# Optimization experiments

Hardware: AMD Instinct MI355X
Metric: run time of the kernel (lower is better)

The kernel has to match this reference:

```python
import jax, jax.numpy as jnp
import numpy as np

EPS = 1e-8


def setup_inputs() -> dict:
    key = jax.random.key(0)
    k1, k2 = jax.random.split(key)
    B, C, L = 16, 4, 4096
    K, S = 256, 128
    x = jax.random.normal(k1, (B, C, L), dtype=jnp.float32)
    shapelets = jax.random.normal(k2, (C, K, S), dtype=jnp.float32)
    return {"x": x, "shapelets": shapelets}


def reference(x, shapelets):
    # x: (B, C, L); shapelets: (C, K, S)
    B, C, L = x.shape
    _, K, S = shapelets.shape
    W = L - S + 1  # number of sliding windows

    # unfold: (B, C, W, S) sliding windows with stride 1
    idx = jnp.arange(W)[:, None] + jnp.arange(S)[None, :]  # (W, S)
    win = x[:, :, idx]  # (B, C, W, S)
    win = win / jnp.maximum(jnp.linalg.norm(win, axis=-1, keepdims=True), EPS)

    shp = shapelets / jnp.maximum(
        jnp.linalg.norm(shapelets, axis=-1, keepdims=True), EPS
    )  # (C, K, S)

    # pairwise dot products: (B, C, W, K)
    sim = jnp.einsum("bcws,cks->bcwk", win, shp)
    # sum over channels, keepdim, transpose(2,3), divide by n_dims
    sim = jnp.sum(sim, axis=1, keepdims=True) / C  # (B, 1, W, K)
    sim = jnp.transpose(sim, (0, 1, 3, 2))  # (B, 1, K, W)
    sim = jax.nn.relu(sim)
    # global max-pool over window positions -> (B, 1, K)
    return jnp.max(sim, axis=3)
```

## Files before the change

### kernel.cpp

```cpp
#include <hip/hip_runtime.h>
#include <hip/hip_bf16.h>

#define NB 16
#define NC 4
#define NL 4096
#define NK 256
#define NS 128
#define NW (NL - NS + 1)
#define WPB 128
#define NWT ((NW + WPB - 1) / WPB)
#define KPB 64
#define EPSF 1e-8f

typedef __attribute__((ext_vector_type(8))) short bf16x8;
typedef __attribute__((ext_vector_type(4))) float floatx4;

typedef __attribute__((address_space(3))) unsigned int* lds_ptr_t;
typedef const __attribute__((address_space(1))) unsigned int* gbl_ptr_t;

__device__ inline short f2bf(float f) {
    __hip_bfloat16 h = __float2bfloat16(f);
    short s;
    __builtin_memcpy(&s, &h, sizeof(short));
    return s;
}

__device__ inline void gload_lds16(const void* g, void* l) {
    __builtin_amdgcn_global_load_lds((gbl_ptr_t)g, (lds_ptr_t)l, 16, 0, 0);
}

__global__ __launch_bounds__(64)
void norm_shp_kernel(const float* __restrict__ shp, short* __restrict__ shpn) {
    int ck = blockIdx.x;
    int k = ck & (NK - 1);
    int lane = threadIdx.x;
    const float* p = shp + (size_t)ck * NS;
    float v0 = p[lane];
    float v1 = p[lane + 64];
    float ss = v0 * v0 + v1 * v1;
    #pragma unroll
    for (int o = 32; o > 0; o >>= 1) ss += __shfl_xor(ss, o, 64);
    float rn = 1.f / fmaxf(sqrtf(ss), EPSF);
    int s0 = lane, s1 = lane + 64;
    int d0 = ((((s0 >> 3) ^ (k & 15)) << 3) | (s0 & 7));
    int d1 = ((((s1 >> 3) ^ (k & 15)) << 3) | (s1 & 7));
    shpn[(size_t)ck * NS + d0] = f2bf(v0 * rn);
    shpn[(size_t)ck * NS + d1] = f2bf(v1 * rn);
}

__global__ __launch_bounds__(256, 2)
void mcs_main_kernel(const float* __restrict__ x,
                     const short* __restrict__ shpn,
                     float* __restrict__ out) {
    __shared__ bf16x8 bs[NC][KPB * 16];
    __shared__ alignas(16) short xcp[NC][4][264];
    __shared__ alignas(16) float scratch[NC][264];
    __shared__ float invw[NC][WPB];

    const int kq = blockIdx.x, slot = blockIdx.y;
    const int tid = threadIdx.x;
    const int lane = tid & 63, wv = tid >> 6;
    const int m = lane & 15, q = lane >> 4, r = m & 3;
    const int kh = wv & 1, wh = wv >> 1;

    float xv[16];
    #pragma unroll
    for (int t = 0; t < 4; t++) {
        const int idx = slot * 4 + t;
        const int wt = idx & 31, b = idx >> 5;
        const int g = wt * WPB + tid;
        #pragma unroll
        for (int c = 0; c < NC; c++)
            xv[t * 4 + c] = (g < NL) ? x[((size_t)b * NC + c) * NL + g] : 0.f;
    }
    {
        const char* gbase = (const char*)shpn + (size_t)(kq * KPB) * NS * 2;
        #pragma unroll
        for (int c = 0; c < NC; c++) {
            const char* gc = gbase + (size_t)c * NK * NS * 2;
            char* lc = (char*)&bs[c][0];
            #pragma unroll
            for (int i = 0; i < 4; i++) {
                int off = (wv * 4 + i) * 1024;
                gload_lds16(gc + off + lane * 16, lc + off);
            }
        }
    }

    float res[4];

    #pragma unroll
    for (int t = 0; t < 4; t++) {
        const int idx = slot * 4 + t;
        const int wt = idx & 31;
        const int w0 = wt * WPB;

        #pragma unroll
        for (int c = 0; c < NC; c++) {
            float xf = xv[t * 4 + c];
            short hv = f2bf(xf);
            #pragma unroll
            for (int rr = 0; rr < 4; rr++) {
                int o2 = tid - rr;
                if (o2 >= 0) xcp[c][rr][o2] = hv;
            }
            scratch[c][tid] = xf * xf;
        }
        __syncthreads();

        {
            float4 v = *(const float4*)&scratch[wv][lane * 4];
            v.y += v.x; v.z += v.y; v.w += v.z;
            float tt = v.w;
            #pragma unroll
            for (int o = 1; o < 64; o <<= 1) {
                float u = __shfl_up(tt, o, 64);
                if (lane >= o) tt += u;
            }
            float excl = tt - v.w;
            v.x += excl; v.y += excl; v.z += excl; v.w += excl;
            *(float4*)&scratch[wv][lane * 4] = v;
        }
        __syncthreads();

        #pragma unroll
        for (int i = 0; i < 2; i++) {
            int ii = tid + 256 * i;
            int c = ii >> 7, o = ii & 127;
            float nn = scratch[c][o + 127] - (o ? scratch[c][o - 1] : 0.f);
            int w = w0 + o;
            invw[c][o] = (w < NW) ? 1.f / fmaxf(sqrtf(fmaxf(nn, 0.f)), EPSF)
                                  : 0.f;
        }
        if (t == 0) asm volatile("s_waitcnt vmcnt(0)" ::: "memory");
        __syncthreads();

        floatx4 tot[4][2];
        #pragma unroll
        for (int mt = 0; mt < 4; mt++)
            #pragma unroll
            for (int kt = 0; kt < 2; kt++)
                tot[mt][kt] = (floatx4){0.f, 0.f, 0.f, 0.f};

        #pragma unroll
        for (int c = 0; c < NC; c++) {
            floatx4 part[4][2];
            #pragma unroll
            for (int s0 = 0; s0 < NS; s0 += 32) {
                bf16x8 a[4];
                #pragma unroll
                for (int mt = 0; mt < 4; mt++) {
                    int ts = wh * 64 + mt * 16 + m + s0 + q * 8;
                    const uint2* pp = (const uint2*)&xcp[c][r][ts - r];
                    union { uint2 uu[2]; bf16x8 v; } cv;
                    cv.uu[0] = pp[0]; cv.uu[1] = pp[1];
                    a[mt] = cv.v;
                }
                int cc = (s0 >> 3) + q;
                #pragma unroll
                for (int kt = 0; kt < 2; kt++) {
                    int k = kh * 32 + kt * 16 + m;
                    bf16x8 bf = bs[c][(k << 4) | (cc ^ m)];
                    #pragma unroll
                    for (int mt = 0; mt < 4; mt++) {
                        part[mt][kt] = (s0 == 0)
                            ? __builtin_amdgcn_mfma_f32_16x16x32_bf16(
                                  a[mt], bf, (floatx4){0.f,0.f,0.f,0.f}, 0,0,0)
                            : __builtin_amdgcn_mfma_f32_16x16x32_bf16(
                                  a[mt], bf, part[mt][kt], 0, 0, 0);
                    }
                }
            }
            #pragma unroll
            for (int mt = 0; mt < 4; mt++) {
                const float4 iv =
                    *(const float4*)&invw[c][wh * 64 + mt * 16 + q * 4];
                floatx4 ivv = (floatx4){iv.x, iv.y, iv.z, iv.w};
                #pragma unroll
                for (int kt = 0; kt < 2; kt++) tot[mt][kt] += ivv * part[mt][kt];
            }
        }

        #pragma unroll
        for (int kt = 0; kt < 2; kt++) {
            floatx4 v0 = tot[0][kt], v1 = tot[1][kt],
                    v2 = tot[2][kt], v3 = tot[3][kt];
            float mx = fmaxf(fmaxf(fmaxf(v0.x, v0.y), fmaxf(v0.z, v0.w)),
                             fmaxf(fmaxf(v1.x, v1.y), fmaxf(v1.z, v1.w)));
            mx = fmaxf(mx, fmaxf(fmaxf(fmaxf(v2.x, v2.y), fmaxf(v2.z, v2.w)),
                                 fmaxf(fmaxf(v3.x, v3.y), fmaxf(v3.z, v3.w))));
            mx = fmaxf(mx, __shfl_xor(mx, 16, 64));
            mx = fmaxf(mx, __shfl_xor(mx, 32, 64));
            if (lane < 16) scratch[wv][kt * 16 + lane] = mx;
        }
        __syncthreads();
        if (tid < 64) {
            int khh = tid >> 5, j = tid & 31;
            float v = fmaxf(scratch[khh][j], scratch[khh + 2][j]);
            res[t] = fmaxf(v, 0.f) * 0.25f;
        }
        __syncthreads();
    }

    if (tid < 64) {
        int khh = tid >> 5, j = tid & 31;
        int kg = kq * KPB + khh * 32 + j;
        #pragma unroll
        for (int t = 0; t < 4; t++) {
            int b = (slot * 4 + t) >> 5;
            atomicMax((int*)out + (size_t)b * NK + kg, __float_as_int(res[t]));
        }
    }
}

extern "C" void kernel_launch(void* const* d_in, const int* in_sizes, int n_in,
                              void* d_out, int out_size, void* d_ws, size_t ws_size,
                              hipStream_t stream) {
    (void)in_sizes; (void)n_in; (void)out_size; (void)ws_size;
    const float* x   = (const float*)d_in[0];
    const float* shp = (const float*)d_in[1];
    float* out = (float*)d_out;

    short* shpn = (short*)d_ws;

    norm_shp_kernel<<<NC * NK, 64, 0, stream>>>(shp, shpn);
    mcs_main_kernel<<<dim3(4, 128), 256, 0, stream>>>(x, shpn, out);
}
```

Baseline: 75.94 us.

## Enlarge block tile to 256 windows × 128 shapelets with 512 threads

After: 98.57 us. 1.3x slower.

```diff
diff --git a/kernel.cpp b/kernel.cpp
--- a/kernel.cpp
+++ b/kernel.cpp
@@ -7,9 +7,10 @@
 #define NK 256
 #define NS 128
 #define NW (NL - NS + 1)
-#define WPB 128
-#define NWT ((NW + WPB - 1) / WPB)
-#define KPB 64
+#define WPB 256
+#define KPB 128
+#define XEL 384
+#define XROW 400
 #define EPSF 1e-8f
 
 typedef __attribute__((ext_vector_type(8))) short bf16x8;
@@ -48,31 +49,23 @@
     shpn[(size_t)ck * NS + d1] = f2bf(v1 * rn);
 }
 
-__global__ __launch_bounds__(256, 2)
+__global__ __launch_bounds__(512, 2)
 void mcs_main_kernel(const float* __restrict__ x,
                      const short* __restrict__ shpn,
                      float* __restrict__ out) {
     __shared__ bf16x8 bs[NC][KPB * 16];
-    __shared__ alignas(16) short xcp[NC][4][264];
-    __shared__ alignas(16) float scratch[NC][264];
+    __shared__ alignas(16) short xcp[NC][4][XROW];
+    __shared__ alignas(16) float scratch[NC][XEL];
     __shared__ float invw[NC][WPB];
+    __shared__ float epi[8][64];
 
     const int kq = blockIdx.x, slot = blockIdx.y;
+    const int b = slot >> 3, wslot = slot & 7;
     const int tid = threadIdx.x;
     const int lane = tid & 63, wv = tid >> 6;
     const int m = lane & 15, q = lane >> 4, r = m & 3;
     const int kh = wv & 1, wh = wv >> 1;
 
-    float xv[16];
-    #pragma unroll
-    for (int t = 0; t < 4; t++) {
-        const int idx = slot * 4 + t;
-        const int wt = idx & 31, b = idx >> 5;
-        const int g = wt * WPB + tid;
-        #pragma unroll
-        for (int c = 0; c < NC; c++)
-            xv[t * 4 + c] = (g < NL) ? x[((size_t)b * NC + c) * NL + g] : 0.f;
-    }
     {
         const char* gbase = (const char*)shpn + (size_t)(kq * KPB) * NS * 2;
         #pragma unroll
@@ -87,46 +80,61 @@
         }
     }
 
-    float res[4];
-
+    float xv[8];
     #pragma unroll
-    for (int t = 0; t < 4; t++) {
-        const int idx = slot * 4 + t;
-        const int wt = idx & 31;
-        const int w0 = wt * WPB;
-
-        #pragma unroll
-        for (int c = 0; c < NC; c++) {
-            float xf = xv[t * 4 + c];
-            short hv = f2bf(xf);
-            #pragma unroll
-            for (int rr = 0; rr < 4; rr++) {
-                int o2 = tid - rr;
-                if (o2 >= 0) xcp[c][rr][o2] = hv;
-            }
-            scratch[c][tid] = xf * xf;
-        }
-        __syncthreads();
-
-        {
-            float4 v = *(const float4*)&scratch[wv][lane * 4];
-            v.y += v.x; v.z += v.y; v.w += v.z;
-            float tt = v.w;
+    for (int t = 0; t < 2; t++) {
+        const int g = (wslot * 2 + t) * WPB + tid;
+        #pragma unroll
+        for (int c = 0; c < NC; c++)
+            xv[t * 4 + c] = (tid < XEL && g < NL)
+                          ? x[((size_t)b * NC + c) * NL + g] : 0.f;
+    }
+
+    float res[2];
+
+    #pragma unroll
+    for (int t = 0; t < 2; t++) {
+        const int w0 = (wslot * 2 + t) * WPB;
+
+        if (tid < XEL) {
+            #pragma unroll
+            for (int c = 0; c < NC; c++) {
+                float xf = xv[t * 4 + c];
+                short hv = f2bf(xf);
+                #pragma unroll
+                for (int rr = 0; rr < 4; rr++) {
+                    int o2 = tid - rr;
+                    if (o2 >= 0) xcp[c][rr][o2] = hv;
+                }
+                scratch[c][tid] = xf * xf;
+            }
+        }
+        __syncthreads();
+
+        if (wv < 4) {
+            const int c = wv;
+            const int base = lane * 6;
+            float v[6];
+            #pragma unroll
+            for (int i = 0; i < 6; i++) v[i] = scratch[c][base + i];
+            #pragma unroll
+            for (int i = 1; i < 6; i++) v[i] += v[i - 1];
+            float tt = v[5];
             #pragma unroll
             for (int o = 1; o < 64; o <<= 1) {
                 float u = __shfl_up(tt, o, 64);
                 if (lane >= o) tt += u;
             }
-            float excl = tt - v.w;
-            v.x += excl; v.y += excl; v.z += excl; v.w += excl;
-            *(float4*)&scratch[wv][lane * 4] = v;
+            float excl = tt - v[5];
+            #pragma unroll
+            for (int i = 0; i < 6; i++) scratch[c][base + i] = v[i] + excl;
         }
         __syncthreads();
 
         #pragma unroll
         for (int i = 0; i < 2; i++) {
-            int ii = tid + 256 * i;
-            int c = ii >> 7, o = ii & 127;
+            int ii = tid + 512 * i;
+            int c = ii >> 8, o = ii & 255;
             float nn = scratch[c][o + 127] - (o ? scratch[c][o - 1] : 0.f);
             int w = w0 + o;
             invw[c][o] = (w < NW) ? 1.f / fmaxf(sqrtf(fmaxf(nn, 0.f)), EPSF)
@@ -135,16 +143,16 @@
         if (t == 0) asm volatile("s_waitcnt vmcnt(0)" ::: "memory");
         __syncthreads();
 
-        floatx4 tot[4][2];
+        floatx4 tot[4][4];
         #pragma unroll
         for (int mt = 0; mt < 4; mt++)
             #pragma unroll
-            for (int kt = 0; kt < 2; kt++)
+            for (int kt = 0; kt < 4; kt++)
                 tot[mt][kt] = (floatx4){0.f, 0.f, 0.f, 0.f};
 
         #pragma unroll
         for (int c = 0; c < NC; c++) {
-            floatx4 part[4][2];
+            floatx4 part[4][4];
             #pragma unroll
             for (int s0 = 0; s0 < NS; s0 += 32) {
                 bf16x8 a[4];
@@ -158,8 +166,8 @@
                 }
                 int cc = (s0 >> 3) + q;
                 #pragma unroll
-                for (int kt = 0; kt < 2; kt++) {
-                    int k = kh * 32 + kt * 16 + m;
+                for (int kt = 0; kt < 4; kt++) {
+                    int k = kh * 64 + kt * 16 + m;
                     bf16x8 bf = bs[c][(k << 4) | (cc ^ m)];
                     #pragma unroll
                     for (int mt = 0; mt < 4; mt++) {
@@ -177,12 +185,12 @@
                     *(const float4*)&invw[c][wh * 64 + mt * 16 + q * 4];
                 floatx4 ivv = (floatx4){iv.x, iv.y, iv.z, iv.w};
                 #pragma unroll
-                for (int kt = 0; kt < 2; kt++) tot[mt][kt] += ivv * part[mt][kt];
-            }
-        }
-
-        #pragma unroll
-        for (int kt = 0; kt < 2; kt++) {
+                for (int kt = 0; kt < 4; kt++) tot[mt][kt] += ivv * part[mt][kt];
+            }
+        }
+
+        #pragma unroll
+        for (int kt = 0; kt < 4; kt++) {
             floatx4 v0 = tot[0][kt], v1 = tot[1][kt],
                     v2 = tot[2][kt], v3 = tot[3][kt];
             float mx = fmaxf(fmaxf(fmaxf(v0.x, v0.y), fmaxf(v0.z, v0.w)),
@@ -191,25 +199,23 @@
                                  fmaxf(fmaxf(v3.x, v3.y), fmaxf(v3.z, v3.w))));
             mx = fmaxf(mx, __shfl_xor(mx, 16, 64));
             mx = fmaxf(mx, __shfl_xor(mx, 32, 64));
-            if (lane < 16) scratch[wv][kt * 16 + lane] = mx;
-        }
-        __syncthreads();
-        if (tid < 64) {
-            int khh = tid >> 5, j = tid & 31;
-            float v = fmaxf(scratch[khh][j], scratch[khh + 2][j]);
+            if (lane < 16) epi[wv][kt * 16 + lane] = mx;
+        }
+        __syncthreads();
+        if (tid < 128) {
+            int kh_ = tid >> 6, j = tid & 63;
+            float v = fmaxf(fmaxf(epi[kh_][j],     epi[kh_ + 2][j]),
+                            fmaxf(epi[kh_ + 4][j], epi[kh_ + 6][j]));
             res[t] = fmaxf(v, 0.f) * 0.25f;
         }
         __syncthreads();
     }
 
-    if (tid < 64) {
-        int khh = tid >> 5, j = tid & 31;
-        int kg = kq * KPB + khh * 32 + j;
-        #pragma unroll
-        for (int t = 0; t < 4; t++) {
-            int b = (slot * 4 + t) >> 5;
+    if (tid < 128) {
+        int kg = kq * KPB + tid;
+        #pragma unroll
+        for (int t = 0; t < 2; t++)
             atomicMax((int*)out + (size_t)b * NK + kg, __float_as_int(res[t]));
-        }
     }
 }
 
@@ -224,5 +230,5 @@
     short* shpn = (short*)d_ws;
 
     norm_shp_kernel<<<NC * NK, 64, 0, stream>>>(shp, shpn);
-    mcs_main_kernel<<<dim3(4, 128), 256, 0, stream>>>(x, shpn, out);
-}
+    mcs_main_kernel<<<dim3(2, 128), 512, 0, stream>>>(x, shpn, out);
+}
```
